# Performance work log

Hardware: AMD Instinct MI355X
Metric: run time of the kernel (lower is better)

## Reference

```python
import jax, jax.numpy as jnp
import numpy as np

B, N, E, H = 4, 2048, 768, 8
D = E // H
SCALING = D ** (-0.5)


def setup_inputs() -> dict:
    key = jax.random.key(0)
    k0, k1, k2, k3, k4 = jax.random.split(key, 5)
    x = jax.random.normal(k0, (B, N, E), dtype=jnp.float32)
    Wqkv = jax.random.normal(k1, (E, 3 * E), dtype=jnp.float32) * 0.02
    bqkv = jax.random.normal(k2, (3 * E,), dtype=jnp.float32) * 0.02
    Wproj = jax.random.normal(k3, (E, E), dtype=jnp.float32) * 0.02
    bproj = jax.random.normal(k4, (E,), dtype=jnp.float32) * 0.02
    return {"x": x, "Wqkv": Wqkv, "bqkv": bqkv, "Wproj": Wproj, "bproj": bproj}


def reference(x, Wqkv, bqkv, Wproj, bproj):
    b, n, e = x.shape
    h, d = H, E // H
    # QKV projection: [b, n, 3e]
    qkv = x @ Wqkv + bqkv
    # rearrange 'b n (h d qkv) -> qkv b h n d': qkv is the INNERMOST axis
    qkv = qkv.reshape(b, n, h, d, 3)
    q = jnp.transpose(qkv[..., 0], (0, 2, 1, 3))  # [b, h, n, d]
    k = jnp.transpose(qkv[..., 1], (0, 2, 1, 3))
    v = jnp.transpose(qkv[..., 2], (0, 2, 1, 3))
    # unscaled attention scores, softmax, then post-softmax scaling (as in source)
    energy = jnp.einsum('bhqd,bhkd->bhqk', q, k)  # [b, h, n, n]
    att = jax.nn.softmax(energy, axis=-1) * SCALING
    out = jnp.einsum('bhqk,bhkd->bhqd', att, v)   # [b, h, n, d]
    out = jnp.transpose(out, (0, 2, 1, 3)).reshape(b, n, e)
    return out @ Wproj + bproj
```

## Files before the change

kernel.cpp:

```cpp
#include <hip/hip_runtime.h>
#include <cstdint>

#define BB 4
#define SEQ 2048
#define EMB 768
#define NH 8
#define HD 96
#define E3 2304
#define MTOK 8192
#define SCALING 0.10206207261596575f
#define LOG2E 1.44269504f

typedef unsigned short u16;
typedef __bf16 bf16x8 __attribute__((ext_vector_type(8)));
typedef float f32x4 __attribute__((ext_vector_type(4)));

__device__ __forceinline__ u16 f2bf(float f) {
    union { float f; uint32_t u; } c; c.f = f;
    uint32_t u = c.u;
    return (u16)((u + 0x7FFFu + ((u >> 16) & 1u)) >> 16);
}
__device__ __forceinline__ u16 f2bf_fast(float f) {
    union { float f; uint32_t u; } c; c.f = f;
    return (u16)((c.u + 0x8000u) >> 16);
}
__device__ __forceinline__ uint32_t pk2(float a, float b) {
    return (uint32_t)f2bf(a) | ((uint32_t)f2bf(b) << 16);
}
__device__ __forceinline__ float fexp2(float x) {
    return __builtin_amdgcn_exp2f(x);
}


__global__ void cvt_x_kernel(const float* __restrict__ src, u16* __restrict__ dst, int n8) {
    int i = blockIdx.x * blockDim.x + threadIdx.x;
    if (i >= n8) return;
    const float4* s4 = (const float4*)src;
    float4 a = s4[2 * i];
    float4 c = s4[2 * i + 1];
    uint4 o;
    o.x = pk2(a.x, a.y); o.y = pk2(a.z, a.w);
    o.z = pk2(c.x, c.y); o.w = pk2(c.z, c.w);
    ((uint4*)dst)[i] = o;
}

__global__ __launch_bounds__(256) void transpose_w_kernel(const float* __restrict__ src,
                                                          u16* __restrict__ dst,
                                                          int ncols, int perm) {
    __shared__ float T[64][65];
    int j0 = blockIdx.x * 64, k0 = blockIdx.y * 64;
    int tid = threadIdx.x;
#pragma unroll
    for (int it = 0; it < 16; ++it) {
        int lin = it * 256 + tid;
        int rr = lin >> 6, jj = lin & 63;
        int j = j0 + jj;
        int c = perm ? (((j % 768) / 96) * 288 + (j % 96) * 3 + (j / 768)) : j;
        T[rr][jj] = src[(k0 + rr) * ncols + c];
    }
    __syncthreads();
#pragma unroll
    for (int it = 0; it < 16; ++it) {
        int lin = it * 256 + tid;
        int jr = lin >> 6, kc = lin & 63;
        dst[(j0 + jr) * 768 + k0 + kc] = f2bf(T[kc][jr]);
    }
}

__global__ void cvt_bias_kernel(const float* __restrict__ bqkv, float* __restrict__ bp) {
    int j = blockIdx.x * blockDim.x + threadIdx.x;
    if (j < E3) {
        int s = j / 768, rr = j % 768, hh = rr / 96, dd = rr % 96;
        bp[j] = bqkv[hh * 288 + dd * 3 + s];
    }
}


__device__ __forceinline__ void gemm_tiles(const u16* __restrict__ A,
                                           const u16* __restrict__ Bt,
                                           int m0, int n0, int tid,
                                           u16* As, u16* Bs, f32x4 acc[4][4]) {
    const int lane = tid & 63;
    const int w = tid >> 6;
    const int l15 = lane & 15;
    const int quad = lane >> 4;
    const int wr = (w >> 1) * 64;
    const int wc = (w & 1) * 64;
    for (int kb = 0; kb < 768; kb += 64) {
#pragma unroll
        for (int it = 0; it < 4; ++it) {
            int ch = it * 256 + tid;
            int row = ch >> 3, cc = ch & 7;
            *(uint4*)&As[row * 72 + cc * 8] = *(const uint4*)&A[(m0 + row) * 768 + kb + cc * 8];
            *(uint4*)&Bs[row * 72 + cc * 8] = *(const uint4*)&Bt[(n0 + row) * 768 + kb + cc * 8];
        }
        __syncthreads();
#pragma unroll
        for (int ks = 0; ks < 2; ++ks) {
            bf16x8 af[4], bfg[4];
#pragma unroll
            for (int fi = 0; fi < 4; ++fi)
                af[fi] = *(const bf16x8*)&As[(wr + fi * 16 + l15) * 72 + ks * 32 + quad * 8];
#pragma unroll
            for (int fj = 0; fj < 4; ++fj)
                bfg[fj] = *(const bf16x8*)&Bs[(wc + fj * 16 + l15) * 72 + ks * 32 + quad * 8];
#pragma unroll
            for (int fi = 0; fi < 4; ++fi)
#pragma unroll
                for (int fj = 0; fj < 4; ++fj)
                    acc[fi][fj] = __builtin_amdgcn_mfma_f32_16x16x32_bf16(af[fi], bfg[fj], acc[fi][fj], 0, 0, 0);
        }
        __syncthreads();
    }
}

__global__ __launch_bounds__(256) void gemm_qkv_kernel(const u16* __restrict__ A,
                                                       const u16* __restrict__ Bt,
                                                       const float* __restrict__ bias,
                                                       u16* __restrict__ qb,
                                                       u16* __restrict__ kb2,
                                                       u16* __restrict__ vb) {
    __shared__ __align__(16) u16 As[128 * 72];
    __shared__ __align__(16) u16 Bs[128 * 72];
    int tid = threadIdx.x;
    int n0 = blockIdx.x * 128, m0 = blockIdx.y * 128;
    f32x4 acc[4][4] = {};
    gemm_tiles(A, Bt, m0, n0, tid, As, Bs, acc);
    int lane = tid & 63, w = tid >> 6, l15 = lane & 15, quad = lane >> 4;
    int wr = (w >> 1) * 64, wc = (w & 1) * 64;
#pragma unroll
    for (int fj = 0; fj < 4; ++fj) {
        int j = n0 + wc + fj * 16 + l15;
        int s = j / 768, rr = j % 768;
        int hh = rr / 96, dd = rr % 96;
        float bv = bias[j];
        float scale = (s == 0) ? LOG2E : 1.0f;
        u16* dstbase = (s == 0) ? qb : (s == 1) ? kb2 : vb;
#pragma unroll
        for (int fi = 0; fi < 4; ++fi) {
#pragma unroll
            for (int r = 0; r < 4; ++r) {
                int m = m0 + wr + fi * 16 + quad * 4 + r;
                int b = m >> 11, n = m & 2047;
                dstbase[((b * NH + hh) * SEQ + n) * HD + dd] = f2bf((acc[fi][fj][r] + bv) * scale);
            }
        }
    }
}

__global__ __launch_bounds__(256) void gemm_proj_kernel(const u16* __restrict__ A,
                                                        const u16* __restrict__ Bt,
                                                        const float* __restrict__ bias,
                                                        float* __restrict__ out) {
    __shared__ __align__(16) u16 As[128 * 72];
    __shared__ __align__(16) u16 Bs[128 * 72];
    int tid = threadIdx.x;
    int n0 = blockIdx.x * 128, m0 = blockIdx.y * 128;
    f32x4 acc[4][4] = {};
    gemm_tiles(A, Bt, m0, n0, tid, As, Bs, acc);
    int lane = tid & 63, w = tid >> 6, l15 = lane & 15, quad = lane >> 4;
    int wr = (w >> 1) * 64, wc = (w & 1) * 64;
#pragma unroll
    for (int fj = 0; fj < 4; ++fj) {
        int j = n0 + wc + fj * 16 + l15;
        float bv = bias[j];
#pragma unroll
        for (int fi = 0; fi < 4; ++fi) {
#pragma unroll
            for (int r = 0; r < 4; ++r) {
                int m = m0 + wr + fi * 16 + quad * 4 + r;
                out[m * 768 + j] = acc[fi][fj][r] + bv;
            }
        }
    }
}

__global__ __launch_bounds__(512) void attn_kernel(const u16* __restrict__ Q,
                                                   const u16* __restrict__ K,
                                                   const u16* __restrict__ V,
                                                   u16* __restrict__ AO) {
    __shared__ __align__(16) u16 Ks[64 * 104];
    __shared__ __align__(16) u16 Vs[96 * 72];
    __shared__ __align__(16) u16 Ps[8][16 * 72];
    int tid = threadIdx.x;
    int lane = tid & 63, w = tid >> 6, l15 = lane & 15, quad = lane >> 4;
    int qt = blockIdx.x, bh = blockIdx.y;
    int b = bh >> 3, h = bh & 7;
    const u16* qp = Q + bh * (SEQ * HD);
    const u16* kp = K + bh * (SEQ * HD);
    const u16* vp = V + bh * (SEQ * HD);
    int q0 = qt * 128;

    bf16x8 aq[3];
#pragma unroll
    for (int ks = 0; ks < 3; ++ks)
        aq[ks] = *(const bf16x8*)&qp[(q0 + w * 16 + l15) * HD + ks * 32 + quad * 8];

    f32x4 O[6] = {};
    float lp[4] = {0.f, 0.f, 0.f, 0.f};

    for (int kt = 0; kt < SEQ / 64; ++kt) {
        int k0 = kt * 64;
        {
            int key = tid / 12 , cc = tid % 12;
            *(uint4*)&Ks[key * 104 + cc * 8] = *(const uint4*)&kp[k0 * HD + tid * 8];
            if (tid < 256) {
                int lin = 512 + tid;
                key = lin / 12; cc = lin % 12;
                *(uint4*)&Ks[key * 104 + cc * 8] = *(const uint4*)&kp[k0 * HD + lin * 8];
            }
        }
        {
            int key = tid & 63, wv = tid >> 6;
#pragma unroll
            for (int it = 0; it < 2; ++it) {
                int cc = it * 8 + wv;
                if (cc < 12) {
                    union { uint4 u; u16 s[8]; } uu;
                    uu.u = *(const uint4*)&vp[(k0 + key) * HD + cc * 8];
#pragma unroll
                    for (int e = 0; e < 8; ++e) Vs[(cc * 8 + e) * 72 + key] = uu.s[e];
                }
            }
        }
        __syncthreads();

        f32x4 S[4] = {};
#pragma unroll
        for (int ks = 0; ks < 3; ++ks) {
            bf16x8 bk[4];
#pragma unroll
            for (int fj = 0; fj < 4; ++fj)
                bk[fj] = *(const bf16x8*)&Ks[(fj * 16 + l15) * 104 + ks * 32 + quad * 8];
#pragma unroll
            for (int fj = 0; fj < 4; ++fj)
                S[fj] = __builtin_amdgcn_mfma_f32_16x16x32_bf16(aq[ks], bk[fj], S[fj], 0, 0, 0);
        }

#pragma unroll
        for (int r = 0; r < 4; ++r) {
            int prow = (quad * 4 + r) * 72;
            float p0 = fexp2(S[0][r]);
            float p1 = fexp2(S[1][r]);
            float p2 = fexp2(S[2][r]);
            float p3 = fexp2(S[3][r]);
            Ps[w][prow + 0 * 16 + l15] = f2bf_fast(p0);
            Ps[w][prow + 1 * 16 + l15] = f2bf_fast(p1);
            Ps[w][prow + 2 * 16 + l15] = f2bf_fast(p2);
            Ps[w][prow + 3 * 16 + l15] = f2bf_fast(p3);
            lp[r] += (p0 + p1) + (p2 + p3);
        }

        bf16x8 ap[2];
#pragma unroll
        for (int ks2 = 0; ks2 < 2; ++ks2)
            ap[ks2] = *(const bf16x8*)&Ps[w][l15 * 72 + ks2 * 32 + quad * 8];
#pragma unroll
        for (int cf = 0; cf < 6; ++cf) {
#pragma unroll
            for (int ks2 = 0; ks2 < 2; ++ks2) {
                bf16x8 vbf = *(const bf16x8*)&Vs[(cf * 16 + l15) * 72 + ks2 * 32 + quad * 8];
                O[cf] = __builtin_amdgcn_mfma_f32_16x16x32_bf16(ap[ks2], vbf, O[cf], 0, 0, 0);
            }
        }
        __syncthreads();
    }

#pragma unroll
    for (int r = 0; r < 4; ++r) {
        float lr = lp[r];
        lr += __shfl_xor(lr, 1);
        lr += __shfl_xor(lr, 2);
        lr += __shfl_xor(lr, 4);
        lr += __shfl_xor(lr, 8);
        float sc = SCALING / lr;
        int n = q0 + w * 16 + quad * 4 + r;
        u16* dst = &AO[(b * SEQ + n) * EMB + h * HD];
#pragma unroll
        for (int cf = 0; cf < 6; ++cf)
            dst[cf * 16 + l15] = f2bf(O[cf][r] * sc);
    }
}


extern "C" void kernel_launch(void* const* d_in, const int* in_sizes, int n_in,
                              void* d_out, int out_size, void* d_ws, size_t ws_size,
                              hipStream_t stream) {
    const float* x     = (const float*)d_in[0];
    const float* Wqkv  = (const float*)d_in[1];
    const float* bqkv  = (const float*)d_in[2];
    const float* Wproj = (const float*)d_in[3];
    const float* bproj = (const float*)d_in[4];
    float* out = (float*)d_out;

    char* p = (char*)d_ws;
    u16*   xb    = (u16*)p;  p += (size_t)MTOK * EMB * 2;
    u16*   wqkvt = (u16*)p;  p += (size_t)E3 * EMB * 2;
    float* bqkvp = (float*)p; p += (size_t)E3 * 4;
    u16*   wpt   = (u16*)p;  p += (size_t)EMB * EMB * 2;
    u16*   qb    = (u16*)p;  p += (size_t)MTOK * EMB * 2;
    u16*   kb    = (u16*)p;  p += (size_t)MTOK * EMB * 2;
    u16*   vb    = (u16*)p;  p += (size_t)MTOK * EMB * 2;
    u16*   ao    = (u16*)p;  p += (size_t)MTOK * EMB * 2;

    cvt_x_kernel<<<MTOK * EMB / 8 / 256, 256, 0, stream>>>(x, xb, MTOK * EMB / 8);
    transpose_w_kernel<<<dim3(E3 / 64, EMB / 64), 256, 0, stream>>>(Wqkv, wqkvt, E3, 1);
    transpose_w_kernel<<<dim3(EMB / 64, EMB / 64), 256, 0, stream>>>(Wproj, wpt, EMB, 0);
    cvt_bias_kernel<<<E3 / 256, 256, 0, stream>>>(bqkv, bqkvp);
    gemm_qkv_kernel<<<dim3(E3 / 128, MTOK / 128), 256, 0, stream>>>(xb, wqkvt, bqkvp, qb, kb, vb);
    attn_kernel<<<dim3(SEQ / 128, BB * NH), 512, 0, stream>>>(qb, kb, vb, ao);
    gemm_proj_kernel<<<dim3(EMB / 128, MTOK / 128), 256, 0, stream>>>(ao, wpt, bproj, out);
}
```

Measured before the change: 260.7 us.

## Use async global-to-LDS loads, swizzled layouts, and 32x32 MFMA attention

Replaces register-staged global-to-LDS copies in the GEMMs and attention with global_load_lds async loads into XOR-swizzled, unpadded LDS tiles. The QKV GEMM epilogue now writes K in a padded swizzled layout and V pre-transposed, so attention no longer scalar-transposes V into shared memory. The attention kernel is rewritten with 32x32x16 MFMAs, 256 threads each handling 32 query rows, and keeps P in registers via a cross-half shuffle instead of round-tripping through LDS. This cuts LDS traffic and bank conflicts at the cost of more complex indexing, scattered epilogue stores, and fewer threads per block.

Result: faster. 250.0 us (-4.1%).

```diff
diff --git a/kernel.cpp b/kernel.cpp
--- a/kernel.cpp
+++ b/kernel.cpp
@@ -12,8 +12,10 @@
 #define LOG2E 1.44269504f
 
 typedef unsigned short u16;
+typedef unsigned int u32;
 typedef __bf16 bf16x8 __attribute__((ext_vector_type(8)));
 typedef float f32x4 __attribute__((ext_vector_type(4)));
+typedef float f32x16 __attribute__((ext_vector_type(16)));
 
 __device__ __forceinline__ u16 f2bf(float f) {
     union { float f; uint32_t u; } c; c.f = f;
@@ -27,8 +29,16 @@
 __device__ __forceinline__ uint32_t pk2(float a, float b) {
     return (uint32_t)f2bf(a) | ((uint32_t)f2bf(b) << 16);
 }
+__device__ __forceinline__ uint32_t pk2_fast(float a, float b) {
+    return (uint32_t)f2bf_fast(a) | ((uint32_t)f2bf_fast(b) << 16);
+}
 __device__ __forceinline__ float fexp2(float x) {
     return __builtin_amdgcn_exp2f(x);
+}
+__device__ __forceinline__ void async16(const u16* g, u16* l) {
+    __builtin_amdgcn_global_load_lds(
+        (const __attribute__((address_space(1))) void*)g,
+        (__attribute__((address_space(3))) void*)l, 16, 0, 0);
 }
 
 
@@ -86,13 +96,16 @@
     const int quad = lane >> 4;
     const int wr = (w >> 1) * 64;
     const int wc = (w & 1) * 64;
+    const int swz = l15 & 7;
     for (int kb = 0; kb < 768; kb += 64) {
 #pragma unroll
         for (int it = 0; it < 4; ++it) {
-            int ch = it * 256 + tid;
-            int row = ch >> 3, cc = ch & 7;
-            *(uint4*)&As[row * 72 + cc * 8] = *(const uint4*)&A[(m0 + row) * 768 + kb + cc * 8];
-            *(uint4*)&Bs[row * 72 + cc * 8] = *(const uint4*)&Bt[(n0 + row) * 768 + kb + cc * 8];
+            int base = (w * 4 + it) * 64;
+            int lin = base + lane;
+            int row = lin >> 3, cl = lin & 7;
+            int cg = cl ^ (row & 7);
+            async16(&A[(size_t)(m0 + row) * 768 + kb + cg * 8], &As[base * 8]);
+            async16(&Bt[(size_t)(n0 + row) * 768 + kb + cg * 8], &Bs[base * 8]);
         }
         __syncthreads();
 #pragma unroll
@@ -100,10 +113,10 @@
             bf16x8 af[4], bfg[4];
 #pragma unroll
             for (int fi = 0; fi < 4; ++fi)
-                af[fi] = *(const bf16x8*)&As[(wr + fi * 16 + l15) * 72 + ks * 32 + quad * 8];
+                af[fi] = *(const bf16x8*)&As[(wr + fi * 16 + l15) * 64 + (((ks * 4 + quad) ^ swz) * 8)];
 #pragma unroll
             for (int fj = 0; fj < 4; ++fj)
-                bfg[fj] = *(const bf16x8*)&Bs[(wc + fj * 16 + l15) * 72 + ks * 32 + quad * 8];
+                bfg[fj] = *(const bf16x8*)&Bs[(wc + fj * 16 + l15) * 64 + (((ks * 4 + quad) ^ swz) * 8)];
 #pragma unroll
             for (int fi = 0; fi < 4; ++fi)
 #pragma unroll
@@ -118,10 +131,10 @@
                                                        const u16* __restrict__ Bt,
                                                        const float* __restrict__ bias,
                                                        u16* __restrict__ qb,
-                                                       u16* __restrict__ kb2,
-                                                       u16* __restrict__ vb) {
-    __shared__ __align__(16) u16 As[128 * 72];
-    __shared__ __align__(16) u16 Bs[128 * 72];
+                                                       u16* __restrict__ kg,
+                                                       u16* __restrict__ vt) {
+    __shared__ __align__(16) u16 As[128 * 64];
+    __shared__ __align__(16) u16 Bs[128 * 64];
     int tid = threadIdx.x;
     int n0 = blockIdx.x * 128, m0 = blockIdx.y * 128;
     f32x4 acc[4][4] = {};
@@ -134,15 +147,23 @@
         int s = j / 768, rr = j % 768;
         int hh = rr / 96, dd = rr % 96;
         float bv = bias[j];
-        float scale = (s == 0) ? LOG2E : 1.0f;
-        u16* dstbase = (s == 0) ? qb : (s == 1) ? kb2 : vb;
 #pragma unroll
         for (int fi = 0; fi < 4; ++fi) {
 #pragma unroll
             for (int r = 0; r < 4; ++r) {
                 int m = m0 + wr + fi * 16 + quad * 4 + r;
                 int b = m >> 11, n = m & 2047;
-                dstbase[((b * NH + hh) * SEQ + n) * HD + dd] = f2bf((acc[fi][fj][r] + bv) * scale);
+                int bh = b * NH + hh;
+                float v = acc[fi][fj][r] + bv;
+                if (s == 0) {
+                    qb[((size_t)bh * SEQ + n) * HD + dd] = f2bf(v * LOG2E);
+                } else if (s == 1) {
+                    int cp = (dd >> 3) ^ (n & 7);
+                    kg[((size_t)bh * SEQ + n) * 128 + cp * 8 + (dd & 7)] = f2bf(v);
+                } else {
+                    int kk = (n & ~63) | ((((n >> 3) ^ dd) & 7) << 3) | (n & 7);
+                    vt[((size_t)bh * HD + dd) * SEQ + kk] = f2bf(v);
+                }
             }
         }
     }
@@ -152,8 +173,8 @@
                                                         const u16* __restrict__ Bt,
                                                         const float* __restrict__ bias,
                                                         float* __restrict__ out) {
-    __shared__ __align__(16) u16 As[128 * 72];
-    __shared__ __align__(16) u16 Bs[128 * 72];
+    __shared__ __align__(16) u16 As[128 * 64];
+    __shared__ __align__(16) u16 Bs[128 * 64];
     int tid = threadIdx.x;
     int n0 = blockIdx.x * 128, m0 = blockIdx.y * 128;
     f32x4 acc[4][4] = {};
@@ -169,116 +190,118 @@
 #pragma unroll
             for (int r = 0; r < 4; ++r) {
                 int m = m0 + wr + fi * 16 + quad * 4 + r;
-                out[m * 768 + j] = acc[fi][fj][r] + bv;
+                out[(size_t)m * 768 + j] = acc[fi][fj][r] + bv;
             }
         }
     }
 }
 
-__global__ __launch_bounds__(512) void attn_kernel(const u16* __restrict__ Q,
-                                                   const u16* __restrict__ K,
-                                                   const u16* __restrict__ V,
+__global__ __launch_bounds__(256) void attn_kernel(const u16* __restrict__ Q,
+                                                   const u16* __restrict__ Kg,
+                                                   const u16* __restrict__ Vt,
                                                    u16* __restrict__ AO) {
-    __shared__ __align__(16) u16 Ks[64 * 104];
-    __shared__ __align__(16) u16 Vs[96 * 72];
-    __shared__ __align__(16) u16 Ps[8][16 * 72];
+    __shared__ __align__(16) u16 Ks[64 * 128];
+    __shared__ __align__(16) u16 Vs[96 * 64];
     int tid = threadIdx.x;
-    int lane = tid & 63, w = tid >> 6, l15 = lane & 15, quad = lane >> 4;
+    int lane = tid & 63, w = tid >> 6;
+    int l31 = lane & 31, hf = lane >> 5;
+    int swz = l31 & 7;
     int qt = blockIdx.x, bh = blockIdx.y;
-    int b = bh >> 3, h = bh & 7;
-    const u16* qp = Q + bh * (SEQ * HD);
-    const u16* kp = K + bh * (SEQ * HD);
-    const u16* vp = V + bh * (SEQ * HD);
-    int q0 = qt * 128;
-
-    bf16x8 aq[3];
-#pragma unroll
-    for (int ks = 0; ks < 3; ++ks)
-        aq[ks] = *(const bf16x8*)&qp[(q0 + w * 16 + l15) * HD + ks * 32 + quad * 8];
-
-    f32x4 O[6] = {};
-    float lp[4] = {0.f, 0.f, 0.f, 0.f};
+    int b = bh >> 3, head = bh & 7;
+    const u16* qp = Q + (size_t)bh * SEQ * HD;
+    const u16* kgp = Kg + (size_t)bh * SEQ * 128;
+    const u16* vtp = Vt + (size_t)bh * HD * SEQ;
+    int q0 = qt * 128 + w * 32;
+
+    bf16x8 aq[6];
+#pragma unroll
+    for (int dc = 0; dc < 6; ++dc)
+        aq[dc] = *(const bf16x8*)&qp[(size_t)(q0 + l31) * HD + dc * 16 + hf * 8];
+
+    f32x16 Ot[3] = {};
+    float lp = 0.f;
 
     for (int kt = 0; kt < SEQ / 64; ++kt) {
         int k0 = kt * 64;
-        {
-            int key = tid / 12 , cc = tid % 12;
-            *(uint4*)&Ks[key * 104 + cc * 8] = *(const uint4*)&kp[k0 * HD + tid * 8];
-            if (tid < 256) {
-                int lin = 512 + tid;
-                key = lin / 12; cc = lin % 12;
-                *(uint4*)&Ks[key * 104 + cc * 8] = *(const uint4*)&kp[k0 * HD + lin * 8];
+#pragma unroll
+        for (int it = 0; it < 4; ++it) {
+            int cw = w * 4 + it;
+            const u16* g = kgp + (size_t)(k0 + cw * 4 + (lane >> 4)) * 128 + (lane & 15) * 8;
+            async16(g, &Ks[cw * 512]);
+        }
+#pragma unroll
+        for (int it = 0; it < 3; ++it) {
+            int vw = w * 3 + it;
+            const u16* g = vtp + (size_t)(vw * 8 + (lane >> 3)) * SEQ + k0 + (lane & 7) * 8;
+            async16(g, &Vs[vw * 512]);
+        }
+        __syncthreads();
+
+        f32x16 Sv[2] = {};
+#pragma unroll
+        for (int tau = 0; tau < 2; ++tau) {
+#pragma unroll
+            for (int dc = 0; dc < 6; ++dc) {
+                bf16x8 ka = *(const bf16x8*)&Ks[(tau * 32 + l31) * 128 + (((2 * dc + hf) ^ swz) * 8)];
+                Sv[tau] = __builtin_amdgcn_mfma_f32_32x32x16_bf16(ka, aq[dc], Sv[tau], 0, 0, 0);
             }
         }
-        {
-            int key = tid & 63, wv = tid >> 6;
-#pragma unroll
-            for (int it = 0; it < 2; ++it) {
-                int cc = it * 8 + wv;
-                if (cc < 12) {
-                    union { uint4 u; u16 s[8]; } uu;
-                    uu.u = *(const uint4*)&vp[(k0 + key) * HD + cc * 8];
-#pragma unroll
-                    for (int e = 0; e < 8; ++e) Vs[(cc * 8 + e) * 72 + key] = uu.s[e];
+
+        u32 pk[2][4][2];
+#pragma unroll
+        for (int tau = 0; tau < 2; ++tau)
+#pragma unroll
+            for (int g = 0; g < 4; ++g)
+#pragma unroll
+                for (int u = 0; u < 2; ++u) {
+                    float p0 = fexp2(Sv[tau][g * 4 + 2 * u]);
+                    float p1 = fexp2(Sv[tau][g * 4 + 2 * u + 1]);
+                    lp += p0 + p1;
+                    pk[tau][g][u] = pk2_fast(p0, p1);
+                }
+        u32 rv[2][2][2];
+#pragma unroll
+        for (int tau = 0; tau < 2; ++tau)
+#pragma unroll
+            for (int kc = 0; kc < 2; ++kc)
+#pragma unroll
+                for (int u = 0; u < 2; ++u) {
+                    u32 send = hf ? pk[tau][2 * kc][u] : pk[tau][2 * kc + 1][u];
+                    rv[tau][kc][u] = (u32)__shfl_xor((int)send, 32);
+                }
+#pragma unroll
+        for (int tau = 0; tau < 2; ++tau) {
+#pragma unroll
+            for (int kc = 0; kc < 2; ++kc) {
+                union { u32 u[4]; bf16x8 v; } pf;
+                pf.u[0] = hf ? rv[tau][kc][0] : pk[tau][2 * kc][0];
+                pf.u[1] = hf ? rv[tau][kc][1] : pk[tau][2 * kc][1];
+                pf.u[2] = hf ? pk[tau][2 * kc + 1][0] : rv[tau][kc][0];
+                pf.u[3] = hf ? pk[tau][2 * kc + 1][1] : rv[tau][kc][1];
+#pragma unroll
+                for (int t = 0; t < 3; ++t) {
+                    bf16x8 va = *(const bf16x8*)&Vs[(t * 32 + l31) * 64 + (((4 * tau + 2 * kc + hf) ^ swz) * 8)];
+                    Ot[t] = __builtin_amdgcn_mfma_f32_32x32x16_bf16(va, pf.v, Ot[t], 0, 0, 0);
                 }
             }
         }
         __syncthreads();
-
-        f32x4 S[4] = {};
-#pragma unroll
-        for (int ks = 0; ks < 3; ++ks) {
-            bf16x8 bk[4];
-#pragma unroll
-            for (int fj = 0; fj < 4; ++fj)
-                bk[fj] = *(const bf16x8*)&Ks[(fj * 16 + l15) * 104 + ks * 32 + quad * 8];
-#pragma unroll
-            for (int fj = 0; fj < 4; ++fj)
-                S[fj] = __builtin_amdgcn_mfma_f32_16x16x32_bf16(aq[ks], bk[fj], S[fj], 0, 0, 0);
-        }
-
-#pragma unroll
-        for (int r = 0; r < 4; ++r) {
-            int prow = (quad * 4 + r) * 72;
-            float p0 = fexp2(S[0][r]);
-            float p1 = fexp2(S[1][r]);
-            float p2 = fexp2(S[2][r]);
-            float p3 = fexp2(S[3][r]);
-            Ps[w][prow + 0 * 16 + l15] = f2bf_fast(p0);
-            Ps[w][prow + 1 * 16 + l15] = f2bf_fast(p1);
-            Ps[w][prow + 2 * 16 + l15] = f2bf_fast(p2);
-            Ps[w][prow + 3 * 16 + l15] = f2bf_fast(p3);
-            lp[r] += (p0 + p1) + (p2 + p3);
-        }
-
-        bf16x8 ap[2];
-#pragma unroll
-        for (int ks2 = 0; ks2 < 2; ++ks2)
-            ap[ks2] = *(const bf16x8*)&Ps[w][l15 * 72 + ks2 * 32 + quad * 8];
-#pragma unroll
-        for (int cf = 0; cf < 6; ++cf) {
-#pragma unroll
-            for (int ks2 = 0; ks2 < 2; ++ks2) {
-                bf16x8 vbf = *(const bf16x8*)&Vs[(cf * 16 + l15) * 72 + ks2 * 32 + quad * 8];
-                O[cf] = __builtin_amdgcn_mfma_f32_16x16x32_bf16(ap[ks2], vbf, O[cf], 0, 0, 0);
-            }
-        }
-        __syncthreads();
-    }
-
-#pragma unroll
-    for (int r = 0; r < 4; ++r) {
-        float lr = lp[r];
-        lr += __shfl_xor(lr, 1);
-        lr += __shfl_xor(lr, 2);
-        lr += __shfl_xor(lr, 4);
-        lr += __shfl_xor(lr, 8);
-        float sc = SCALING / lr;
-        int n = q0 + w * 16 + quad * 4 + r;
-        u16* dst = &AO[(b * SEQ + n) * EMB + h * HD];
-#pragma unroll
-        for (int cf = 0; cf < 6; ++cf)
-            dst[cf * 16 + l15] = f2bf(O[cf][r] * sc);
+    }
+
+    float l = lp + __shfl_xor(lp, 32);
+    float sc = SCALING / l;
+    int n = q0 + l31;
+    size_t rowbase = ((size_t)b * SEQ + n) * EMB + head * HD;
+#pragma unroll
+    for (int t = 0; t < 3; ++t) {
+#pragma unroll
+        for (int g = 0; g < 4; ++g) {
+            int d0 = t * 32 + 8 * g + 4 * hf;
+            uint2 val;
+            val.x = pk2(Ot[t][g * 4 + 0] * sc, Ot[t][g * 4 + 1] * sc);
+            val.y = pk2(Ot[t][g * 4 + 2] * sc, Ot[t][g * 4 + 3] * sc);
+            *(uint2*)&AO[rowbase + d0] = val;
+        }
     }
 }
 
@@ -299,15 +322,15 @@
     float* bqkvp = (float*)p; p += (size_t)E3 * 4;
     u16*   wpt   = (u16*)p;  p += (size_t)EMB * EMB * 2;
     u16*   qb    = (u16*)p;  p += (size_t)MTOK * EMB * 2;
-    u16*   kb    = (u16*)p;  p += (size_t)MTOK * EMB * 2;
-    u16*   vb    = (u16*)p;  p += (size_t)MTOK * EMB * 2;
+    u16*   kg    = (u16*)p;  p += (size_t)BB * NH * SEQ * 128 * 2;
+    u16*   vt    = (u16*)p;  p += (size_t)MTOK * EMB * 2;
     u16*   ao    = (u16*)p;  p += (size_t)MTOK * EMB * 2;
 
     cvt_x_kernel<<<MTOK * EMB / 8 / 256, 256, 0, stream>>>(x, xb, MTOK * EMB / 8);
     transpose_w_kernel<<<dim3(E3 / 64, EMB / 64), 256, 0, stream>>>(Wqkv, wqkvt, E3, 1);
     transpose_w_kernel<<<dim3(EMB / 64, EMB / 64), 256, 0, stream>>>(Wproj, wpt, EMB, 0);
     cvt_bias_kernel<<<E3 / 256, 256, 0, stream>>>(bqkv, bqkvp);
-    gemm_qkv_kernel<<<dim3(E3 / 128, MTOK / 128), 256, 0, stream>>>(xb, wqkvt, bqkvp, qb, kb, vb);
-    attn_kernel<<<dim3(SEQ / 128, BB * NH), 512, 0, stream>>>(qb, kb, vb, ao);
+    gemm_qkv_kernel<<<dim3(E3 / 128, MTOK / 128), 256, 0, stream>>>(xb, wqkvt, bqkvp, qb, kg, vt);
+    attn_kernel<<<dim3(SEQ / 128, BB * NH), 256, 0, stream>>>(qb, kg, vt, ao);
     gemm_proj_kernel<<<dim3(EMB / 128, MTOK / 128), 256, 0, stream>>>(ao, wpt, bproj, out);
 }
```
